# Performance work log

Measured on AMD Instinct MI355X. Metric: run time of the kernel, lower is better.

The kernel has to match this reference:

```python
import jax, jax.numpy as jnp
import numpy as np

K_BITS = 8
QMAX = float(2 ** (K_BITS - 1) - 1)  # 127 for symmetric int8 fake quant
BN_EPS = 1e-5
RES_SCALE = 1.0


def _ste(v, q):
    # straight-through estimator: forward q, backward identity wrt v
    return v + jax.lax.stop_gradient(q - v)


def quant_act(x, alpha):
    # PAMS-style: clamp to learnable alpha, symmetric uniform fake-quant
    xc = jnp.clip(x, -alpha, alpha)
    scale = alpha / QMAX
    q = jnp.round(xc / scale) * scale
    return _ste(xc, q)


def quant_weight(w):
    # symmetric max-abs weight fake-quant
    scale = jnp.max(jnp.abs(w)) / QMAX
    q = jnp.clip(jnp.round(w / scale), -QMAX, QMAX) * scale
    return _ste(w, q)


def conv3x3(x, w):
    return jax.lax.conv_general_dilated(
        x, w, window_strides=(1, 1), padding=[(1, 1), (1, 1)],
        dimension_numbers=("NCHW", "OIHW", "NCHW"))


def batchnorm(x, gamma, beta):
    # training-mode BN: biased batch statistics over (N, H, W)
    mean = jnp.mean(x, axis=(0, 2, 3), keepdims=True)
    var = jnp.var(x, axis=(0, 2, 3), keepdims=True)
    xhat = (x - mean) * jax.lax.rsqrt(var + BN_EPS)
    return xhat * gamma[None, :, None, None] + beta[None, :, None, None]


def prelu(x, a):
    return jnp.where(x >= 0, x, a * x)


def setup_inputs() -> dict:
    key = jax.random.key(0)
    ks = jax.random.split(key, 4)
    C = 64
    identity = jax.random.normal(ks[0], (8, C, 192, 192), dtype=jnp.float32)
    # conv weights, default_init_weights scale 0.1 (kaiming-ish * 0.1)
    w1 = jax.random.normal(ks[1], (C, C, 3, 3), dtype=jnp.float32) * 0.1
    w2 = jax.random.normal(ks[2], (C, C, 3, 3), dtype=jnp.float32) * 0.1
    return {
        "identity": identity,
        "bits": jnp.ones((1,), jnp.float32),
        "f": jnp.ones((1,), jnp.float32),
        "bits_out": jnp.zeros((1,), jnp.float32),
        "w1": w1,
        "w2": w2,
        "alpha1": jnp.array(8.0, jnp.float32),
        "alpha2": jnp.array(8.0, jnp.float32),
        "gamma1": jnp.ones((C,), jnp.float32),
        "beta1": jnp.zeros((C,), jnp.float32),
        "gamma2": jnp.ones((C,), jnp.float32),
        "beta2": jnp.zeros((C,), jnp.float32),
        "prelu_a": jnp.array(0.25, jnp.float32),
        "shortcut": jnp.ones((1,), jnp.float32),
    }


def reference(identity, bits, f, bits_out, w1, w2, alpha1, alpha2,
              gamma1, beta1, gamma2, beta2, prelu_a, shortcut):
    # quant conv1: quantize input act + weights, 3x3 conv
    x = conv3x3(quant_act(identity, alpha1), quant_weight(w1))
    # PReLU then BN1 (module applies bn1(act(x)))
    x = batchnorm(prelu(x, prelu_a), gamma1, beta1)
    # quant conv2
    out = conv3x3(quant_act(x, alpha2), quant_weight(w2))
    out = batchnorm(out, gamma2, beta2)
    out = identity * shortcut + out * RES_SCALE
    return (out, bits, f, bits_out)
```

## Files before the change

### kernel.cpp

```cpp
#include <hip/hip_runtime.h>
#include <hip/hip_bf16.h>
#include <math.h>

#define CNUM   64
#define HH     192
#define WW     192
#define NBATCH 8
#define HWSZ   (HH * WW)
#define CHWSZ  (CNUM * HWSZ)
#define TOTALSZ ((size_t)NBATCH * CHWSZ)
#define QMAXF  127.0f
#define BNEPS  1e-5f
#define PW     194

typedef __attribute__((ext_vector_type(4))) int i32x4;

#define OFF_PK1    0
#define OFF_PK2    18432
#define OFF_STATS  36864
#define OFF_SUM1   36864
#define OFF_SSQ1   37120
#define OFF_SUM2   37376
#define OFF_SSQ2   37632
#define OFF_WMAX   37888
#define OFF_SW     37890
#define OFF_QA     38148
#define OFF_QB     (38148 + 9634816)

__device__ inline void gload16(const void* g, void* l) {
    __builtin_amdgcn_global_load_lds(
        (const __attribute__((address_space(1))) unsigned int*)g,
        (__attribute__((address_space(3))) unsigned int*)l, 16, 0, 0);
}
__device__ inline float bf2f(unsigned short u) {
    return __builtin_bit_cast(float, (unsigned)u << 16);
}

__global__ __launch_bounds__(256)
void wmax_kernel(const float* __restrict__ w1,
                 const float* __restrict__ w2,
                 unsigned* __restrict__ wmaxbits) {
    const int which = blockIdx.y;
    const float4* w4 = (const float4*)(which ? w2 : w1);
    const int b = (blockIdx.x * 256 + threadIdx.x) * 2;
    const float4 a = w4[b], c = w4[b + 1];
    float m = fmaxf(fmaxf(fmaxf(fabsf(a.x), fabsf(a.y)), fmaxf(fabsf(a.z), fabsf(a.w))),
                    fmaxf(fmaxf(fabsf(c.x), fabsf(c.y)), fmaxf(fabsf(c.z), fabsf(c.w))));
#pragma unroll
    for (int off = 1; off < 64; off <<= 1) m = fmaxf(m, __shfl_xor(m, off));
    if ((threadIdx.x & 63) == 0)
        atomicMax(wmaxbits + which, __builtin_bit_cast(unsigned, m));
}

__global__ __launch_bounds__(256)
void wpack_kernel(const float* __restrict__ w1,
                  const float* __restrict__ w2,
                  const unsigned* __restrict__ wmaxbits,
                  char* __restrict__ pk1,
                  char* __restrict__ pk2,
                  float* __restrict__ swout) {
    const int which = blockIdx.y;
    const float* w  = which ? w2 : w1;
    char*        pk = which ? pk2 : pk1;
    const float scale = __builtin_bit_cast(float, wmaxbits[which]) / QMAXF;
    if (blockIdx.x == 0 && threadIdx.x == 0) swout[which] = scale;
    const int i0 = (blockIdx.x * 256 + threadIdx.x) * 8;
#pragma unroll
    for (int k = 0; k < 8; ++k) {
        const int i = i0 + k;
        const int j   = i & 15;
        const int l   = (i >> 4) & 63;
        const int ocb = (i >> 10) & 3;
        const int t   = i >> 12;
        const int oc  = ocb * 16 + (l & 15);
        const int ic  = ((l >> 4) & 3) * 16 + j;
        float q = rintf(w[oc * 576 + ic * 9 + t] / scale);
        q = fminf(fmaxf(q, -QMAXF), QMAXF);
        pk[i] = (char)(int)q;
    }
}

__global__ __launch_bounds__(256)
void requant_kernel(const float* __restrict__ inp,
                    const float* __restrict__ alpha_p,
                    char* __restrict__ q) {
    const int tid  = threadIdx.x;
    const int xblk = blockIdx.x;
    const int pr   = blockIdx.y;
    const int n    = blockIdx.z;
    const int x0   = xblk * 64;
    const float alpha  = alpha_p[0];
    const float inv_qs = QMAXF / alpha;

    __shared__ char s[2][64 * 76];

    const int xq  = tid & 15;
    const int icl = tid >> 4;

    float4 r[2][4];
    bool inter[2];
#pragma unroll
    for (int h = 0; h < 2; ++h) {
        const int py = 2 * pr + h;
        inter[h] = (py >= 1 && py <= 192);
        if (inter[h]) {
            const int gy = py - 1;
#pragma unroll
            for (int p = 0; p < 4; ++p) {
                const int ic = icl * 4 + p;
                const size_t fo = ((size_t)n * CNUM + ic) * HWSZ + (size_t)gy * WW + x0 + xq * 4;
                r[h][p] = *(const float4*)(inp + fo);
            }
        }
    }

#pragma unroll
    for (int h = 0; h < 2; ++h) {
        if (inter[h]) {
#pragma unroll
            for (int j = 0; j < 4; ++j) {
                unsigned pk = 0;
#pragma unroll
                for (int p = 0; p < 4; ++p) {
                    const float* rv = (const float*)&r[h][p];
                    float v = fminf(fmaxf(rv[j], -alpha), alpha);
                    v = rintf(v * inv_qs);
                    pk |= ((unsigned)(unsigned char)(char)(int)v) << (8 * p);
                }
                *(unsigned*)&s[h][(xq * 4 + j) * 76 + icl * 4] = pk;
            }
        }
    }
    __syncthreads();

    const int xx = tid >> 2;
    const int g  = tid & 3;
#pragma unroll
    for (int h = 0; h < 2; ++h) {
        const int py = 2 * pr + h;
        char* qrow = q + ((size_t)n * PW + py) * (PW * 64);
        if (py == 0 || py == PW - 1) {
            for (int i = xblk * 256 + tid; i < PW * 4; i += 768)
                ((int4*)qrow)[i] = make_int4(0, 0, 0, 0);
            continue;
        }
        if (xblk == 0 && tid < 4) ((int4*)qrow)[tid] = make_int4(0, 0, 0, 0);
        if (xblk == 2 && tid < 4) ((int4*)(qrow + 193 * 64))[tid] = make_int4(0, 0, 0, 0);

        const int px = 1 + x0 + xx;
        const int gp = g ^ ((px >> 1) & 3);
        const unsigned* sp = (const unsigned*)&s[h][xx * 76 + g * 16];
        int4 val;
        val.x = (int)sp[0]; val.y = (int)sp[1]; val.z = (int)sp[2]; val.w = (int)sp[3];
        *(int4*)(qrow + (size_t)px * 64 + gp * 16) = val;
    }
}

template<int XFORM, int SWZOUT>
__global__ __launch_bounds__(256, 3)
void conv_mfma_kernel(const char* __restrict__ q,
                      const char* __restrict__ wpk,
                      const float* __restrict__ swp,
                      const float* __restrict__ alpha_p,
                      const float* __restrict__ slope_p,
                      const float* __restrict__ st_sum,
                      const float* __restrict__ st_ssq,
                      const float* __restrict__ st_gamma,
                      const float* __restrict__ st_beta,
                      unsigned short* __restrict__ outp,
                      unsigned short* __restrict__ out_swz,
                      float* __restrict__ sum_g,
                      float* __restrict__ ssq_g) {
    __shared__ __align__(16) char s_in[1584 * 16];
    __shared__ __align__(16) short sT[SWZOUT ? 4 * 64 * 40 : 8];
    __shared__ float sred[256], ssred[256];
    __shared__ float sab[128];

    const int tid = threadIdx.x;
    const int x0 = blockIdx.x * 64;
    const int y0 = blockIdx.y * 4;
    const int n  = blockIdx.z;

    const float alpha  = alpha_p[0];
    const float inv_qs = QMAXF / alpha;

    if (XFORM) {
        if (tid < 64) {
            const float cnt = (float)(NBATCH * HWSZ);
            const float sm = st_sum[tid] + st_sum[64 + tid] + st_sum[128 + tid] + st_sum[192 + tid];
            const float sq = st_ssq[tid] + st_ssq[64 + tid] + st_ssq[128 + tid] + st_ssq[192 + tid];
            const float mean = sm / cnt;
            const float var  = sq / cnt - mean * mean;
            const float inv  = 1.0f / sqrtf(var + BNEPS);
            const float a = st_gamma[tid] * inv;
            sab[tid] = a;
            sab[64 + tid] = st_beta[tid] - mean * a;
        }
        __syncthreads();
        const unsigned short* qv = (const unsigned short*)q;
        const unsigned short* qb0 = qv + ((size_t)(n * PW + y0) * PW + x0) * 64;
#pragma unroll
        for (int k = 0; k < 7; ++k) {
            const int c = tid + k * 256;
            if (c < 1584) {
                const int r  = c / 264;
                const int w  = c - r * 264;
                const int x  = w >> 2, gp = w & 3;
                const int px = x0 + x, pyy = y0 + r;
                int4 val = make_int4(0, 0, 0, 0);
                if ((unsigned)(px - 1) < 192u && (unsigned)(pyy - 1) < 192u) {
                    const int g16 = gp ^ ((x >> 1) & 3);
                    const unsigned short* qp = qb0 + (size_t)r * (PW * 64) + (size_t)x * 64;
                    const int s0 = (2 * g16) ^ (px & 7);
                    const int4 v0 = *(const int4*)(qp + s0 * 8);
                    const int4 v1 = *(const int4*)(qp + (s0 ^ 1) * 8);
                    const unsigned short* u0 = (const unsigned short*)&v0;
                    const unsigned short* u1 = (const unsigned short*)&v1;
                    char vb[16];
#pragma unroll
                    for (int jj = 0; jj < 8; ++jj) {
                        const int ic = g16 * 16 + jj;
                        float xx0 = sab[ic] * bf2f(u0[jj]) + sab[64 + ic];
                        xx0 = fminf(fmaxf(xx0, -alpha), alpha);
                        vb[jj] = (char)(int)rintf(xx0 * inv_qs);
                    }
#pragma unroll
                    for (int jj = 0; jj < 8; ++jj) {
                        const int ic = g16 * 16 + 8 + jj;
                        float xx1 = sab[ic] * bf2f(u1[jj]) + sab[64 + ic];
                        xx1 = fminf(fmaxf(xx1, -alpha), alpha);
                        vb[8 + jj] = (char)(int)rintf(xx1 * inv_qs);
                    }
                    val = *(int4*)vb;
                }
                *(int4*)&s_in[c * 16] = val;
            }
        }
    } else {
        const char* g0 = q + ((size_t)(n * PW + y0) * PW + x0) * 64;
        for (int c = tid; c < 1584; c += 256) {
            const int r = c / 264;
            const int w = c - r * 264;
            gload16(g0 + (size_t)r * (PW * 64) + w * 16, &s_in[c * 16]);
        }
    }
    __syncthreads();

    const int wave  = tid >> 6;
    const int lane  = tid & 63;
    const int xlane = lane & 15;
    const int icgl  = lane >> 4;

    i32x4 acc[4][4];
#pragma unroll
    for (int m = 0; m < 4; ++m)
#pragma unroll
        for (int nb = 0; nb < 4; ++nb) acc[m][nb] = (i32x4){0, 0, 0, 0};

#pragma unroll
    for (int t = 0; t < 9; ++t) {
        const int ky = t / 3, kx = t % 3;
        const int r = wave + ky;
        i32x4 bfrag[4], afrag[4];
        const char* bp = wpk + ((size_t)(t * 4) * 64 + lane) * 16;
#pragma unroll
        for (int nb = 0; nb < 4; ++nb) bfrag[nb] = *(const i32x4*)(bp + (size_t)nb * 1024);
#pragma unroll
        for (int m = 0; m < 4; ++m) {
            const int x = m * 16 + xlane + kx;
            afrag[m] = *(const i32x4*)&s_in[(size_t)((r * 66 + x) * 4 + (icgl ^ ((x >> 1) & 3))) * 16];
        }
#pragma unroll
        for (int m = 0; m < 4; ++m)
#pragma unroll
            for (int nb = 0; nb < 4; ++nb)
                acc[m][nb] = __builtin_amdgcn_mfma_i32_16x16x64_i8(
                    afrag[m], bfrag[nb], acc[m][nb], 0, 0, 0);
    }

    const float sfin  = (alpha / QMAXF) * swp[0];
    const float slope = slope_p ? slope_p[0] : 1.0f;
    const int gy  = y0 + wave;
    const int gx0 = x0 + icgl * 4;

    if (SWZOUT) {
#pragma unroll
        for (int h = 0; h < 2; ++h) {
#pragma unroll
            for (int nbi = 0; nbi < 2; ++nbi) {
                const int nb = 2 * h + nbi;
                const int oc = nb * 16 + xlane;
                float s = 0.0f, ss = 0.0f;
#pragma unroll
                for (int m = 0; m < 4; ++m) {
#pragma unroll
                    for (int rgi = 0; rgi < 4; ++rgi) {
                        float a = (float)acc[m][nb][rgi] * sfin;
                        a = (a >= 0.0f) ? a : slope * a;
                        s += a;
                        ss += a * a;
                        const int pxl = m * 16 + icgl * 4 + rgi;
                        sT[(wave * 64 + pxl) * 40 + (nbi * 16 + xlane)] =
                            (short)__builtin_bit_cast(unsigned short, __float2bfloat16(a));
                    }
                }
                s  += __shfl_xor(s, 16);  s  += __shfl_xor(s, 32);
                ss += __shfl_xor(ss, 16); ss += __shfl_xor(ss, 32);
                if (icgl == 0) { sred[wave * 64 + oc] = s; ssred[wave * 64 + oc] = ss; }
            }
            __syncthreads();
            {
                const int py = gy + 1;
                unsigned short* qrow = out_swz + ((size_t)n * PW + py) * (PW * 64);
#pragma unroll
                for (int kk = 0; kk < 4; ++kk) {
                    const int idx = kk * 64 + lane;
                    const int xx  = idx >> 2;
                    const int gg  = idx & 3;
                    const int g8  = h * 4 + gg;
                    const int px  = x0 + 1 + xx;
                    const int slot = g8 ^ (px & 7);
                    *(int4*)(qrow + (size_t)px * 64 + slot * 8) =
                        *(const int4*)&sT[(wave * 64 + xx) * 40 + gg * 8];
                }
            }
            __syncthreads();
        }
    } else {
#pragma unroll
        for (int nb = 0; nb < 4; ++nb) {
            const int oc = nb * 16 + xlane;
            float s = 0.0f, ss = 0.0f;
#pragma unroll
            for (int m = 0; m < 4; ++m) {
                float v[4];
#pragma unroll
                for (int rgi = 0; rgi < 4; ++rgi) {
                    float a = (float)acc[m][nb][rgi] * sfin;
                    a = (a >= 0.0f) ? a : slope * a;
                    v[rgi] = a;
                    s += a;
                    ss += a * a;
                }
                ushort4 pk;
                pk.x = __builtin_bit_cast(unsigned short, __float2bfloat16(v[0]));
                pk.y = __builtin_bit_cast(unsigned short, __float2bfloat16(v[1]));
                pk.z = __builtin_bit_cast(unsigned short, __float2bfloat16(v[2]));
                pk.w = __builtin_bit_cast(unsigned short, __float2bfloat16(v[3]));
                *(ushort4*)&outp[(size_t)(n * CNUM + oc) * HWSZ + (size_t)gy * WW + gx0 + m * 16] = pk;
            }
            s  += __shfl_xor(s, 16);  s  += __shfl_xor(s, 32);
            ss += __shfl_xor(ss, 16); ss += __shfl_xor(ss, 32);
            if (icgl == 0) { sred[wave * 64 + oc] = s; ssred[wave * 64 + oc] = ss; }
        }
        __syncthreads();
    }

    const int bank = (blockIdx.y ^ blockIdx.z) & 3;
    if (tid < 64) {
        atomicAdd(sum_g + bank * 64 + tid,
                  sred[tid] + sred[64 + tid] + sred[128 + tid] + sred[192 + tid]);
    } else if (tid < 128) {
        const int c = tid - 64;
        atomicAdd(ssq_g + bank * 64 + c,
                  ssred[c] + ssred[64 + c] + ssred[128 + c] + ssred[192 + c]);
    }
}

__global__ __launch_bounds__(256)
void final_kernel(const float* __restrict__ identity,
                  const unsigned short* __restrict__ t2,
                  const float* __restrict__ st_sum,
                  const float* __restrict__ st_ssq,
                  const float* __restrict__ st_gamma,
                  const float* __restrict__ st_beta,
                  const float* __restrict__ shortcut_p,
                  const float* __restrict__ bits,
                  const float* __restrict__ f,
                  const float* __restrict__ bits_out,
                  float* __restrict__ out) {
    __shared__ float sab[128];
    if (threadIdx.x < 64) {
        const int c = threadIdx.x;
        const float cnt = (float)(NBATCH * HWSZ);
        const float sm = st_sum[c] + st_sum[64 + c] + st_sum[128 + c] + st_sum[192 + c];
        const float sq = st_ssq[c] + st_ssq[64 + c] + st_ssq[128 + c] + st_ssq[192 + c];
        const float mean = sm / cnt;
        const float var  = sq / cnt - mean * mean;
        const float inv  = 1.0f / sqrtf(var + BNEPS);
        const float a = st_gamma[c] * inv;
        sab[c] = a;
        sab[64 + c] = st_beta[c] - mean * a;
    }
    __syncthreads();

    const size_t base = (size_t)blockIdx.x * 1024;
    const int   cch  = (int)((base / (HWSZ / 4)) % CNUM);
    const float a  = sab[cch];
    const float bb = sab[64 + cch];
    const float sc = shortcut_p[0];

    float4  idv[4];
    ushort4 tv[4];
#pragma unroll
    for (int k = 0; k < 4; ++k) {
        const size_t i4 = base + (size_t)k * 256 + threadIdx.x;
        idv[k] = ((const float4*)identity)[i4];
        tv[k]  = ((const ushort4*)t2)[i4];
    }
#pragma unroll
    for (int k = 0; k < 4; ++k) {
        const size_t i4 = base + (size_t)k * 256 + threadIdx.x;
        float4 o;
        o.x = idv[k].x * sc + a * bf2f(tv[k].x) + bb;
        o.y = idv[k].y * sc + a * bf2f(tv[k].y) + bb;
        o.z = idv[k].z * sc + a * bf2f(tv[k].z) + bb;
        o.w = idv[k].w * sc + a * bf2f(tv[k].w) + bb;
        ((float4*)out)[i4] = o;
    }
    if (blockIdx.x == 0 && threadIdx.x == 0) {
        out[TOTALSZ + 0] = bits[0];
        out[TOTALSZ + 1] = f[0];
        out[TOTALSZ + 2] = bits_out[0];
    }
}

extern "C" void kernel_launch(void* const* d_in, const int* in_sizes, int n_in,
                              void* d_out, int out_size, void* d_ws, size_t ws_size,
                              hipStream_t stream) {
    const float* identity = (const float*)d_in[0];
    const float* bits     = (const float*)d_in[1];
    const float* f        = (const float*)d_in[2];
    const float* bits_out = (const float*)d_in[3];
    const float* w1       = (const float*)d_in[4];
    const float* w2       = (const float*)d_in[5];
    const float* alpha1   = (const float*)d_in[6];
    const float* alpha2   = (const float*)d_in[7];
    const float* gamma1   = (const float*)d_in[8];
    const float* beta1    = (const float*)d_in[9];
    const float* gamma2   = (const float*)d_in[10];
    const float* beta2    = (const float*)d_in[11];
    const float* prelu_a  = (const float*)d_in[12];
    const float* shortcut = (const float*)d_in[13];
    float* out = (float*)d_out;
    float* ws  = (float*)d_ws;

    char*     pk1   = (char*)(ws + OFF_PK1);
    char*     pk2   = (char*)(ws + OFF_PK2);
    float*    sum1  = ws + OFF_SUM1;
    float*    ssq1  = ws + OFF_SSQ1;
    float*    sum2  = ws + OFF_SUM2;
    float*    ssq2  = ws + OFF_SSQ2;
    unsigned* wmaxb = (unsigned*)(ws + OFF_WMAX);
    float*    sw    = ws + OFF_SW;
    char*           qa = (char*)(ws + OFF_QA);
    unsigned short* qb = (unsigned short*)(ws + OFF_QB);
    unsigned short* t2 = (unsigned short*)(ws + OFF_QA);

    hipMemsetAsync(ws + OFF_STATS, 0, 1026 * sizeof(float), stream);
    hipLaunchKernelGGL(wmax_kernel, dim3(18, 2), dim3(256), 0, stream, w1, w2, wmaxb);
    hipLaunchKernelGGL(requant_kernel, dim3(3, (PW + 1) / 2, NBATCH), dim3(256), 0, stream,
                       identity, alpha1, qa);
    hipLaunchKernelGGL(wpack_kernel, dim3(18, 2), dim3(256), 0, stream,
                       w1, w2, wmaxb, pk1, pk2, sw);
    hipLaunchKernelGGL((conv_mfma_kernel<0, 1>), dim3(3, HH / 4, NBATCH), dim3(256), 0, stream,
                       qa, pk1, sw + 0, alpha1, prelu_a,
                       (const float*)nullptr, (const float*)nullptr,
                       (const float*)nullptr, (const float*)nullptr,
                       (unsigned short*)nullptr, qb, sum1, ssq1);
    hipLaunchKernelGGL((conv_mfma_kernel<1, 0>), dim3(3, HH / 4, NBATCH), dim3(256), 0, stream,
                       (const char*)qb, pk2, sw + 1, alpha2, (const float*)nullptr,
                       sum1, ssq1, gamma1, beta1,
                       t2, (unsigned short*)nullptr, sum2, ssq2);
    hipLaunchKernelGGL(final_kernel, dim3((unsigned)(TOTALSZ / 4 / 1024)), dim3(256), 0, stream,
                       identity, t2, sum2, ssq2, gamma2, beta2,
                       shortcut, bits, f, bits_out, out);
}
```

Measured before the change: 250.1 us.

## Drop epilogue barriers, use per-wave banked stat atomics, batch input loads

The conv epilogue no longer reduces BN statistics through shared memory. Each wave now shuffle-reduces its own sums and issues atomics into 8 banks, so the two __syncthreads per half-tile and the final one are removed. Each wave's transpose buffer region is private, so it writes and reads it without a block barrier. In the transform variant, all global loads of the bf16 input are issued into registers before the dequant/requant loop to raise memory-level parallelism, at the cost of more registers and more atomics per block.

```diff
diff --git a/kernel.cpp b/kernel.cpp
--- a/kernel.cpp
+++ b/kernel.cpp
@@ -12,6 +12,7 @@
 #define QMAXF  127.0f
 #define BNEPS  1e-5f
 #define PW     194
+#define NBANK  8
 
 typedef __attribute__((ext_vector_type(4))) int i32x4;
 
@@ -19,13 +20,13 @@
 #define OFF_PK2    18432
 #define OFF_STATS  36864
 #define OFF_SUM1   36864
-#define OFF_SSQ1   37120
-#define OFF_SUM2   37376
-#define OFF_SSQ2   37632
-#define OFF_WMAX   37888
-#define OFF_SW     37890
-#define OFF_QA     38148
-#define OFF_QB     (38148 + 9634816)
+#define OFF_SSQ1   37376
+#define OFF_SUM2   37888
+#define OFF_SSQ2   38400
+#define OFF_WMAX   38912
+#define OFF_SW     38914
+#define OFF_QA     38920
+#define OFF_QB     (OFF_QA + 9437184)
 
 __device__ inline void gload16(const void* g, void* l) {
     __builtin_amdgcn_global_load_lds(
@@ -34,6 +35,9 @@
 }
 __device__ inline float bf2f(unsigned short u) {
     return __builtin_bit_cast(float, (unsigned)u << 16);
+}
+__device__ inline short f2bf(float v) {
+    return (short)__builtin_bit_cast(unsigned short, __float2bfloat16(v));
 }
 
 __global__ __launch_bounds__(256)
@@ -173,8 +177,7 @@
                       float* __restrict__ ssq_g) {
     __shared__ __align__(16) char s_in[1584 * 16];
     __shared__ __align__(16) short sT[SWZOUT ? 4 * 64 * 40 : 8];
-    __shared__ float sred[256], ssred[256];
-    __shared__ float sab[128];
+    __shared__ float sab[XFORM ? 128 : 4];
 
     const int tid = threadIdx.x;
     const int x0 = blockIdx.x * 64;
@@ -187,8 +190,12 @@
     if (XFORM) {
         if (tid < 64) {
             const float cnt = (float)(NBATCH * HWSZ);
-            const float sm = st_sum[tid] + st_sum[64 + tid] + st_sum[128 + tid] + st_sum[192 + tid];
-            const float sq = st_ssq[tid] + st_ssq[64 + tid] + st_ssq[128 + tid] + st_ssq[192 + tid];
+            float sm = 0.f, sq = 0.f;
+#pragma unroll
+            for (int k = 0; k < NBANK; ++k) {
+                sm += st_sum[64 * k + tid];
+                sq += st_ssq[64 * k + tid];
+            }
             const float mean = sm / cnt;
             const float var  = sq / cnt - mean * mean;
             const float inv  = 1.0f / sqrtf(var + BNEPS);
@@ -199,6 +206,24 @@
         __syncthreads();
         const unsigned short* qv = (const unsigned short*)q;
         const unsigned short* qb0 = qv + ((size_t)(n * PW + y0) * PW + x0) * 64;
+        int4 v0a[7], v1a[7];
+#pragma unroll
+        for (int k = 0; k < 7; ++k) {
+            const int c = tid + k * 256;
+            if (c < 1584) {
+                const int r  = c / 264;
+                const int w  = c - r * 264;
+                const int x  = w >> 2, gp = w & 3;
+                const int px = x0 + x, pyy = y0 + r;
+                if ((unsigned)(px - 1) < 192u && (unsigned)(pyy - 1) < 192u) {
+                    const int g16 = gp ^ ((x >> 1) & 3);
+                    const unsigned short* qp = qb0 + (size_t)r * (PW * 64) + (size_t)x * 64;
+                    const int s0 = (2 * g16) ^ (px & 7);
+                    v0a[k] = *(const int4*)(qp + s0 * 8);
+                    v1a[k] = *(const int4*)(qp + (s0 ^ 1) * 8);
+                }
+            }
+        }
 #pragma unroll
         for (int k = 0; k < 7; ++k) {
             const int c = tid + k * 256;
@@ -210,12 +235,8 @@
                 int4 val = make_int4(0, 0, 0, 0);
                 if ((unsigned)(px - 1) < 192u && (unsigned)(pyy - 1) < 192u) {
                     const int g16 = gp ^ ((x >> 1) & 3);
-                    const unsigned short* qp = qb0 + (size_t)r * (PW * 64) + (size_t)x * 64;
-                    const int s0 = (2 * g16) ^ (px & 7);
-                    const int4 v0 = *(const int4*)(qp + s0 * 8);
-                    const int4 v1 = *(const int4*)(qp + (s0 ^ 1) * 8);
-                    const unsigned short* u0 = (const unsigned short*)&v0;
-                    const unsigned short* u1 = (const unsigned short*)&v1;
+                    const unsigned short* u0 = (const unsigned short*)&v0a[k];
+                    const unsigned short* u1 = (const unsigned short*)&v1a[k];
                     char vb[16];
 #pragma unroll
                     for (int jj = 0; jj < 8; ++jj) {
@@ -283,54 +304,46 @@
     const int gy  = y0 + wave;
     const int gx0 = x0 + icgl * 4;
 
+    float st_s[4]  = {0.f, 0.f, 0.f, 0.f};
+    float st_ss[4] = {0.f, 0.f, 0.f, 0.f};
+
     if (SWZOUT) {
+        const int py = gy + 1;
+        unsigned short* qrow = out_swz + ((size_t)n * PW + py) * (PW * 64);
 #pragma unroll
         for (int h = 0; h < 2; ++h) {
 #pragma unroll
             for (int nbi = 0; nbi < 2; ++nbi) {
                 const int nb = 2 * h + nbi;
-                const int oc = nb * 16 + xlane;
-                float s = 0.0f, ss = 0.0f;
 #pragma unroll
                 for (int m = 0; m < 4; ++m) {
 #pragma unroll
                     for (int rgi = 0; rgi < 4; ++rgi) {
                         float a = (float)acc[m][nb][rgi] * sfin;
                         a = (a >= 0.0f) ? a : slope * a;
-                        s += a;
-                        ss += a * a;
+                        st_s[nb]  += a;
+                        st_ss[nb] += a * a;
                         const int pxl = m * 16 + icgl * 4 + rgi;
-                        sT[(wave * 64 + pxl) * 40 + (nbi * 16 + xlane)] =
-                            (short)__builtin_bit_cast(unsigned short, __float2bfloat16(a));
+                        sT[(wave * 64 + pxl) * 40 + (nbi * 16 + xlane)] = f2bf(a);
                     }
                 }
-                s  += __shfl_xor(s, 16);  s  += __shfl_xor(s, 32);
-                ss += __shfl_xor(ss, 16); ss += __shfl_xor(ss, 32);
-                if (icgl == 0) { sred[wave * 64 + oc] = s; ssred[wave * 64 + oc] = ss; }
-            }
-            __syncthreads();
-            {
-                const int py = gy + 1;
-                unsigned short* qrow = out_swz + ((size_t)n * PW + py) * (PW * 64);
-#pragma unroll
-                for (int kk = 0; kk < 4; ++kk) {
-                    const int idx = kk * 64 + lane;
-                    const int xx  = idx >> 2;
-                    const int gg  = idx & 3;
-                    const int g8  = h * 4 + gg;
-                    const int px  = x0 + 1 + xx;
-                    const int slot = g8 ^ (px & 7);
-                    *(int4*)(qrow + (size_t)px * 64 + slot * 8) =
-                        *(const int4*)&sT[(wave * 64 + xx) * 40 + gg * 8];
-                }
-            }
-            __syncthreads();
+            }
+#pragma unroll
+            for (int kk = 0; kk < 4; ++kk) {
+                const int idx = kk * 64 + lane;
+                const int xx  = idx >> 2;
+                const int gg  = idx & 3;
+                const int g8  = h * 4 + gg;
+                const int px  = x0 + 1 + xx;
+                const int slot = g8 ^ (px & 7);
+                *(int4*)(qrow + (size_t)px * 64 + slot * 8) =
+                    *(const int4*)&sT[(wave * 64 + xx) * 40 + gg * 8];
+            }
         }
     } else {
 #pragma unroll
         for (int nb = 0; nb < 4; ++nb) {
             const int oc = nb * 16 + xlane;
-            float s = 0.0f, ss = 0.0f;
 #pragma unroll
             for (int m = 0; m < 4; ++m) {
                 float v[4];
@@ -339,31 +352,30 @@
                     float a = (float)acc[m][nb][rgi] * sfin;
                     a = (a >= 0.0f) ? a : slope * a;
                     v[rgi] = a;
-                    s += a;
-                    ss += a * a;
+                    st_s[nb]  += a;
+                    st_ss[nb] += a * a;
                 }
                 ushort4 pk;
-                pk.x = __builtin_bit_cast(unsigned short, __float2bfloat16(v[0]));
-                pk.y = __builtin_bit_cast(unsigned short, __float2bfloat16(v[1]));
-                pk.z = __builtin_bit_cast(unsigned short, __float2bfloat16(v[2]));
-                pk.w = __builtin_bit_cast(unsigned short, __float2bfloat16(v[3]));
+                pk.x = (unsigned short)f2bf(v[0]);
+                pk.y = (unsigned short)f2bf(v[1]);
+                pk.z = (unsigned short)f2bf(v[2]);
+                pk.w = (unsigned short)f2bf(v[3]);
                 *(ushort4*)&outp[(size_t)(n * CNUM + oc) * HWSZ + (size_t)gy * WW + gx0 + m * 16] = pk;
             }
-            s  += __shfl_xor(s, 16);  s  += __shfl_xor(s, 32);
-            ss += __shfl_xor(ss, 16); ss += __shfl_xor(ss, 32);
-            if (icgl == 0) { sred[wave * 64 + oc] = s; ssred[wave * 64 + oc] = ss; }
-        }
-        __syncthreads();
-    }
-
-    const int bank = (blockIdx.y ^ blockIdx.z) & 3;
-    if (tid < 64) {
-        atomicAdd(sum_g + bank * 64 + tid,
-                  sred[tid] + sred[64 + tid] + sred[128 + tid] + sred[192 + tid]);
-    } else if (tid < 128) {
-        const int c = tid - 64;
-        atomicAdd(ssq_g + bank * 64 + c,
-                  ssred[c] + ssred[64 + c] + ssred[128 + c] + ssred[192 + c]);
+        }
+    }
+
+    const int bank = wave + ((blockIdx.y & 1) << 2);
+#pragma unroll
+    for (int nb = 0; nb < 4; ++nb) {
+        float s = st_s[nb], ss = st_ss[nb];
+        s  += __shfl_xor(s, 16);  s  += __shfl_xor(s, 32);
+        ss += __shfl_xor(ss, 16); ss += __shfl_xor(ss, 32);
+        if (icgl == 0) {
+            const int oc = nb * 16 + xlane;
+            atomicAdd(sum_g + bank * 64 + oc, s);
+            atomicAdd(ssq_g + bank * 64 + oc, ss);
+        }
     }
 }
 
@@ -383,8 +395,12 @@
     if (threadIdx.x < 64) {
         const int c = threadIdx.x;
         const float cnt = (float)(NBATCH * HWSZ);
-        const float sm = st_sum[c] + st_sum[64 + c] + st_sum[128 + c] + st_sum[192 + c];
-        const float sq = st_ssq[c] + st_ssq[64 + c] + st_ssq[128 + c] + st_ssq[192 + c];
+        float sm = 0.f, sq = 0.f;
+#pragma unroll
+        for (int k = 0; k < NBANK; ++k) {
+            sm += st_sum[64 * k + c];
+            sq += st_ssq[64 * k + c];
+        }
         const float mean = sm / cnt;
         const float var  = sq / cnt - mean * mean;
         const float inv  = 1.0f / sqrtf(var + BNEPS);
@@ -457,7 +473,7 @@
     unsigned short* qb = (unsigned short*)(ws + OFF_QB);
     unsigned short* t2 = (unsigned short*)(ws + OFF_QA);
 
-    hipMemsetAsync(ws + OFF_STATS, 0, 1026 * sizeof(float), stream);
+    hipMemsetAsync(ws + OFF_STATS, 0, 2052 * sizeof(float), stream);
     hipLaunchKernelGGL(wmax_kernel, dim3(18, 2), dim3(256), 0, stream, w1, w2, wmaxb);
     hipLaunchKernelGGL(requant_kernel, dim3(3, (PW + 1) / 2, NBATCH), dim3(256), 0, stream,
                        identity, alpha1, qa);
```

New measurement: 260.1 us. 1.04x slower.
